# Performance work log

Measured on AMD Instinct MI355X. Metric: run time of the kernel, lower is better.

The kernel has to match this reference:

```python
import jax, jax.numpy as jnp
import numpy as np

N_NODES = 20000
N_EDGES = 320000
IN_F = 168
HID = 256


def gcn_conv(x, W, b, src, dst, ew, n_nodes):
    """PyG GCNConv: symmetric normalization with self-loops (fill 1.0).
    out = D^-1/2 (A + I) D^-1/2 X W^T + b, aggregated at dst (source_to_target).
    """
    xw = x @ W.T  # [N, F_out]
    # degree at target nodes, including self-loop weight 1.0
    deg = jax.ops.segment_sum(ew, dst, num_segments=n_nodes) + 1.0
    dinv = jnp.where(deg > 0, jax.lax.rsqrt(deg), 0.0)
    norm = dinv[src] * ew * dinv[dst]  # [E]
    agg = jax.ops.segment_sum(norm[:, None] * xw[src], dst, num_segments=n_nodes)
    # self-loop contribution: norm_ii = dinv[i]^2
    out = agg + (dinv * dinv)[:, None] * xw
    return out + b


def setup_inputs() -> dict:
    key = jax.random.key(0)
    k = jax.random.split(key, 8)
    x = jax.random.normal(k[0], (N_NODES, IN_F), dtype=jnp.float32)
    edge_index = jax.random.randint(k[1], (2, N_EDGES), 0, N_NODES, dtype=jnp.int64)
    edge_weight = jax.random.uniform(k[2], (N_EDGES,), dtype=jnp.float32)
    # GCN layer weights (PyG Linear: y = x W^T), plus per-layer bias
    s1 = 1.0 / np.sqrt(IN_F)
    s2 = 1.0 / np.sqrt(HID)
    W1 = jax.random.uniform(k[3], (HID, IN_F), minval=-s1, maxval=s1, dtype=jnp.float32)
    b1 = jnp.zeros((HID,), dtype=jnp.float32)
    W2 = jax.random.uniform(k[4], (HID, HID), minval=-s2, maxval=s2, dtype=jnp.float32)
    b2 = jnp.zeros((HID,), dtype=jnp.float32)
    return {"x": x, "edge_index": edge_index, "edge_weight": edge_weight,
            "W1": W1, "b1": b1, "W2": W2, "b2": b2}


def reference(x, edge_index, edge_weight, W1, b1, W2, b2):
    src, dst = edge_index[0], edge_index[1]
    h = gcn_conv(x, W1, b1, src, dst, edge_weight, N_NODES)
    h = jax.nn.relu(h)
    h = gcn_conv(h, W2, b2, src, dst, edge_weight, N_NODES)
    h = jax.nn.relu(h)
    return h
```

## Files before the change

kernel.cpp:

```cpp
#include <hip/hip_runtime.h>

#define N_NODES 20000
#define N_EDGES 320000
#define IN_F    168
#define HID     256
#define K1P     192
#define XS      192
#define NF4     42
#define X4      48

typedef __attribute__((ext_vector_type(8))) short bf16x8;
typedef __attribute__((ext_vector_type(4))) float f32x4;
typedef __attribute__((ext_vector_type(2))) float f32x2;

__device__ __forceinline__ short f2bf(float f) {
    union { float f; unsigned u; } v; v.f = f;
    unsigned r = v.u + 0x7FFFu + ((v.u >> 16) & 1u);
    return (short)(r >> 16);
}
__device__ __forceinline__ f32x2 bfp(unsigned u) {
    f32x2 r;
    r.x = __uint_as_float(u << 16);
    r.y = __uint_as_float(u & 0xFFFF0000u);
    return r;
}

__global__ void prep_all(const float* __restrict__ x, short* __restrict__ xb,
                         const float* __restrict__ W1, const float* __restrict__ W2,
                         short* __restrict__ w1b, short* __restrict__ w2b,
                         const int* __restrict__ ei, const float* __restrict__ ew,
                         float* __restrict__ deg, int* __restrict__ counts) {
    const int xTot  = N_NODES * X4;
    const int w1Tot = 256 * X4;
    const int w2Tot = 256 * 64;
    int i = blockIdx.x * 256 + threadIdx.x;
    if (i < xTot) {
        int n  = i / X4;
        int k4 = i - n * X4;
        short4 o;
        if (k4 < NF4) {
            float4 v = *(const float4*)(x + (size_t)n * IN_F + k4 * 4);
            o = make_short4(f2bf(v.x), f2bf(v.y), f2bf(v.z), f2bf(v.w));
        } else {
            o = make_short4(0, 0, 0, 0);
        }
        *(short4*)(xb + (size_t)n * XS + k4 * 4) = o;
        return;
    }
    i -= xTot;
    if (i < w1Tot) {
        int r  = i / X4;
        int k4 = i - r * X4;
        short4 o;
        if (k4 < NF4) {
            float4 v = *(const float4*)(W1 + (size_t)r * IN_F + k4 * 4);
            o = make_short4(f2bf(v.x), f2bf(v.y), f2bf(v.z), f2bf(v.w));
        } else {
            o = make_short4(0, 0, 0, 0);
        }
        *(short4*)(w1b + (size_t)r * K1P + k4 * 4) = o;
        return;
    }
    i -= w1Tot;
    if (i < w2Tot) {
        int r  = i >> 6;
        int c4 = i & 63;
        float4 v = *(const float4*)(W2 + (size_t)r * HID + c4 * 4);
        *(short4*)(w2b + (size_t)r * HID + c4 * 4) =
            make_short4(f2bf(v.x), f2bf(v.y), f2bf(v.z), f2bf(v.w));
        return;
    }
    i -= w2Tot;
    if (i < N_EDGES) {
        int d = ei[N_EDGES + i];
        atomicAdd(&deg[d], ew[i]);
        atomicAdd(&counts[d], 1);
    }
}


__global__ __launch_bounds__(1024) void scan_part(const int* __restrict__ counts,
                                                  int* __restrict__ offs,
                                                  int* __restrict__ bsum,
                                                  float* __restrict__ deg, int n) {
    int tid  = threadIdx.x;
    int lane = tid & 63;
    int wv   = tid >> 6;
    int i = blockIdx.x * 1024 + tid;
    if (i < n) deg[i] = rsqrtf(deg[i] + 1.0f);
    __shared__ int wsum[16];
    int v = (i < n) ? ((counts[i] + 7) & ~7) : 0;
    int incl = v;
    #pragma unroll
    for (int d = 1; d < 64; d <<= 1) {
        int t = __shfl_up(incl, d);
        if (lane >= d) incl += t;
    }
    if (lane == 63) wsum[wv] = incl;
    __syncthreads();
    if (wv == 0) {
        int w = (lane < 16) ? wsum[lane] : 0;
        int winc = w;
        #pragma unroll
        for (int d = 1; d < 16; d <<= 1) {
            int t = __shfl_up(winc, d);
            if (lane >= d) winc += t;
        }
        if (lane < 16) wsum[lane] = winc - w;
    }
    __syncthreads();
    if (i < n) offs[i] = wsum[wv] + incl - v;
    if (tid == 1023) bsum[blockIdx.x] = wsum[15] + incl;
}

__global__ __launch_bounds__(1024) void scan_add(const int* __restrict__ bsum,
                                                 int* __restrict__ offs, int n) {
    int i = blockIdx.x * 1024 + threadIdx.x;
    int add = 0;
    for (int b = 0; b < (int)blockIdx.x; ++b) add += bsum[b];
    if (i < n) offs[i] += add;
    if (i == n) offs[n] = add + bsum[blockIdx.x];
}

__global__ void scatter_edges(const int* __restrict__ ei, const float* __restrict__ ew,
                              const float* __restrict__ dinv, const int* __restrict__ offs,
                              const int* __restrict__ counts,
                              int* __restrict__ cursor, int2* __restrict__ er) {
    int t = blockIdx.x * 256 + threadIdx.x;
    if (t < N_EDGES) {
        int s = ei[t];
        int d = ei[N_EDGES + t];
        int pos = offs[d] + atomicAdd(&cursor[d], 1);
        float nm = dinv[s] * ew[t] * dinv[d];
        er[pos] = make_int2(s, __float_as_int(nm));
        return;
    }
    int n = t - N_EDGES;
    if (n < N_NODES) {
        int p   = offs[n] + counts[n];
        int end = offs[n + 1];
        for (; p < end; ++p) er[p] = make_int2(0, 0);
    }
}


__global__ __launch_bounds__(256) void agg_x(const short* __restrict__ xb,
                                             const float* __restrict__ dinv,
                                             const int* __restrict__ offs,
                                             const int2* __restrict__ er,
                                             short* __restrict__ ax) {
    int wave = threadIdx.x >> 6;
    int lane = threadIdx.x & 63;
    int n = blockIdx.x * 4 + wave;
    bool act = lane < NF4;
    int lo4 = act ? lane * 4 : 0;
    float di = dinv[n];
    float sw = di * di;
    uint2 sv = *(const uint2*)(xb + (size_t)n * XS + lo4);
    f32x2 a01 = bfp(sv.x) * sw;
    f32x2 a23 = bfp(sv.y) * sw;

    int p0 = offs[n], p1 = offs[n + 1];
    for (int p = p0; p < p1; p += 8) {
        const int4* e4 = (const int4*)(er + p);
        int4 eA = e4[0], eB = e4[1], eC = e4[2], eD = e4[3];
        uint2 r0 = *(const uint2*)(xb + (size_t)eA.x * XS + lo4);
        uint2 r1 = *(const uint2*)(xb + (size_t)eA.z * XS + lo4);
        uint2 r2 = *(const uint2*)(xb + (size_t)eB.x * XS + lo4);
        uint2 r3 = *(const uint2*)(xb + (size_t)eB.z * XS + lo4);
        uint2 r4 = *(const uint2*)(xb + (size_t)eC.x * XS + lo4);
        uint2 r5 = *(const uint2*)(xb + (size_t)eC.z * XS + lo4);
        uint2 r6 = *(const uint2*)(xb + (size_t)eD.x * XS + lo4);
        uint2 r7 = *(const uint2*)(xb + (size_t)eD.z * XS + lo4);
        float w0 = __int_as_float(eA.y), w1 = __int_as_float(eA.w);
        float w2 = __int_as_float(eB.y), w3 = __int_as_float(eB.w);
        float w4 = __int_as_float(eC.y), w5 = __int_as_float(eC.w);
        float w6 = __int_as_float(eD.y), w7 = __int_as_float(eD.w);
        a01 += bfp(r0.x) * w0; a23 += bfp(r0.y) * w0;
        a01 += bfp(r1.x) * w1; a23 += bfp(r1.y) * w1;
        a01 += bfp(r2.x) * w2; a23 += bfp(r2.y) * w2;
        a01 += bfp(r3.x) * w3; a23 += bfp(r3.y) * w3;
        a01 += bfp(r4.x) * w4; a23 += bfp(r4.y) * w4;
        a01 += bfp(r5.x) * w5; a23 += bfp(r5.y) * w5;
        a01 += bfp(r6.x) * w6; a23 += bfp(r6.y) * w6;
        a01 += bfp(r7.x) * w7; a23 += bfp(r7.y) * w7;
    }

    size_t base = (size_t)n * K1P + lane * 4;
    if (act) {
        *(short4*)&ax[base] = make_short4(f2bf(a01.x), f2bf(a01.y),
                                          f2bf(a23.x), f2bf(a23.y));
    } else if (lane < 48) {
        *(short4*)&ax[base] = make_short4(0, 0, 0, 0);
    }
}

__global__ __launch_bounds__(256) void agg_h(const short* __restrict__ h1h,
                                             const float* __restrict__ dinv,
                                             const int* __restrict__ offs,
                                             const int2* __restrict__ er,
                                             short* __restrict__ ah) {
    int wave = threadIdx.x >> 6;
    int lane = threadIdx.x & 63;
    int n = blockIdx.x * 4 + wave;
    int lo4 = lane * 4;
    float di = dinv[n];
    float sw = di * di;
    uint2 sv = *(const uint2*)(h1h + (size_t)n * HID + lo4);
    f32x2 a01 = bfp(sv.x) * sw;
    f32x2 a23 = bfp(sv.y) * sw;

    int p0 = offs[n], p1 = offs[n + 1];
    for (int p = p0; p < p1; p += 8) {
        const int4* e4 = (const int4*)(er + p);
        int4 eA = e4[0], eB = e4[1], eC = e4[2], eD = e4[3];
        uint2 r0 = *(const uint2*)(h1h + (size_t)eA.x * HID + lo4);
        uint2 r1 = *(const uint2*)(h1h + (size_t)eA.z * HID + lo4);
        uint2 r2 = *(const uint2*)(h1h + (size_t)eB.x * HID + lo4);
        uint2 r3 = *(const uint2*)(h1h + (size_t)eB.z * HID + lo4);
        uint2 r4 = *(const uint2*)(h1h + (size_t)eC.x * HID + lo4);
        uint2 r5 = *(const uint2*)(h1h + (size_t)eC.z * HID + lo4);
        uint2 r6 = *(const uint2*)(h1h + (size_t)eD.x * HID + lo4);
        uint2 r7 = *(const uint2*)(h1h + (size_t)eD.z * HID + lo4);
        float w0 = __int_as_float(eA.y), w1 = __int_as_float(eA.w);
        float w2 = __int_as_float(eB.y), w3 = __int_as_float(eB.w);
        float w4 = __int_as_float(eC.y), w5 = __int_as_float(eC.w);
        float w6 = __int_as_float(eD.y), w7 = __int_as_float(eD.w);
        a01 += bfp(r0.x) * w0; a23 += bfp(r0.y) * w0;
        a01 += bfp(r1.x) * w1; a23 += bfp(r1.y) * w1;
        a01 += bfp(r2.x) * w2; a23 += bfp(r2.y) * w2;
        a01 += bfp(r3.x) * w3; a23 += bfp(r3.y) * w3;
        a01 += bfp(r4.x) * w4; a23 += bfp(r4.y) * w4;
        a01 += bfp(r5.x) * w5; a23 += bfp(r5.y) * w5;
        a01 += bfp(r6.x) * w6; a23 += bfp(r6.y) * w6;
        a01 += bfp(r7.x) * w7; a23 += bfp(r7.y) * w7;
    }

    *(short4*)&ah[(size_t)n * HID + lo4] = make_short4(f2bf(a01.x), f2bf(a01.y),
                                                       f2bf(a23.x), f2bf(a23.y));
}


#define LDS_STRIDE 72

__global__ __launch_bounds__(256) void gemm_bf(const short* __restrict__ Ah,
                                               const short* __restrict__ Wh,
                                               const float* __restrict__ bias,
                                               float* __restrict__ Cf,
                                               short* __restrict__ Cbf,
                                               int M, int Ks, int nsteps, int mode) {
    __shared__ short sAh[64 * LDS_STRIDE];
    __shared__ short sWh[64 * LDS_STRIDE];

    const int idx   = blockIdx.x;
    const int group = idx >> 5;
    const int xcd   = idx & 7;
    const int slot  = (idx >> 3) & 3;
    const int mt    = group * 8 + xcd;
    const int mtiles = (M + 63) >> 6;
    if (mt >= mtiles) return;
    const int bm = mt * 64;
    const int bn = slot * 64;

    const int tid  = threadIdx.x;
    const int lane = tid & 63;
    const int wv   = tid >> 6;
    const int l16  = lane & 15;
    const int quad = lane >> 4;
    const int wm   = (wv & 1) * 32;
    const int wn   = (wv >> 1) * 32;

    const int srow = tid >> 2;
    const int sseg = (tid & 3) * 16;
    int arow = bm + srow; if (arow >= M) arow = M - 1;
    const short* gAh = Ah + (size_t)arow * Ks;
    const short* gWh = Wh + (size_t)(bn + srow) * Ks;
    const int lds_off = srow * LDS_STRIDE + sseg;

    f32x4 acc00 = {0,0,0,0}, acc01 = {0,0,0,0}, acc10 = {0,0,0,0}, acc11 = {0,0,0,0};

    int4 pah0 = *(const int4*)(gAh + sseg), pah1 = *(const int4*)(gAh + sseg + 8);
    int4 pwh0 = *(const int4*)(gWh + sseg), pwh1 = *(const int4*)(gWh + sseg + 8);

    for (int ks = 0; ks < nsteps; ++ks) {
        *(int4*)&sAh[lds_off] = pah0; *(int4*)&sAh[lds_off + 8] = pah1;
        *(int4*)&sWh[lds_off] = pwh0; *(int4*)&sWh[lds_off + 8] = pwh1;
        __syncthreads();
        if (ks + 1 < nsteps) {
            int o = (ks + 1) * 64 + sseg;
            pah0 = *(const int4*)(gAh + o); pah1 = *(const int4*)(gAh + o + 8);
            pwh0 = *(const int4*)(gWh + o); pwh1 = *(const int4*)(gWh + o + 8);
        }
        #pragma unroll
        for (int o = 0; o < 2; ++o) {
            const int a0 = (wm + l16) * LDS_STRIDE + o * 32 + quad * 8;
            const int a1 = a0 + 16 * LDS_STRIDE;
            const int w0 = (wn + l16) * LDS_STRIDE + o * 32 + quad * 8;
            const int w1 = w0 + 16 * LDS_STRIDE;
            bf16x8 ah0 = *(const bf16x8*)&sAh[a0];
            bf16x8 ah1 = *(const bf16x8*)&sAh[a1];
            bf16x8 wh0 = *(const bf16x8*)&sWh[w0];
            bf16x8 wh1 = *(const bf16x8*)&sWh[w1];
            acc00 = __builtin_amdgcn_mfma_f32_16x16x32_bf16(ah0, wh0, acc00, 0, 0, 0);
            acc01 = __builtin_amdgcn_mfma_f32_16x16x32_bf16(ah0, wh1, acc01, 0, 0, 0);
            acc10 = __builtin_amdgcn_mfma_f32_16x16x32_bf16(ah1, wh0, acc10, 0, 0, 0);
            acc11 = __builtin_amdgcn_mfma_f32_16x16x32_bf16(ah1, wh1, acc11, 0, 0, 0);
        }
        __syncthreads();
    }

    const int colb = bn + wn + l16;
    const int rowb = bm + wm + quad * 4;
    const float b0 = bias[colb];
    const float b1 = bias[colb + 16];
    #pragma unroll
    for (int r = 0; r < 4; ++r) {
        int row = rowb + r;
        if (row < M) {
            float v0 = acc00[r] + b0; v0 = v0 > 0.f ? v0 : 0.f;
            float v1 = acc01[r] + b1; v1 = v1 > 0.f ? v1 : 0.f;
            if (mode == 0) {
                Cbf[(size_t)row * HID + colb]      = f2bf(v0);
                Cbf[(size_t)row * HID + colb + 16] = f2bf(v1);
            } else {
                Cf[(size_t)row * HID + colb]      = v0;
                Cf[(size_t)row * HID + colb + 16] = v1;
            }
        }
        int row2 = row + 16;
        if (row2 < M) {
            float v0 = acc10[r] + b0; v0 = v0 > 0.f ? v0 : 0.f;
            float v1 = acc11[r] + b1; v1 = v1 > 0.f ? v1 : 0.f;
            if (mode == 0) {
                Cbf[(size_t)row2 * HID + colb]      = f2bf(v0);
                Cbf[(size_t)row2 * HID + colb + 16] = f2bf(v1);
            } else {
                Cf[(size_t)row2 * HID + colb]      = v0;
                Cf[(size_t)row2 * HID + colb + 16] = v1;
            }
        }
    }
}


extern "C" void kernel_launch(void* const* d_in, const int* in_sizes, int n_in,
                              void* d_out, int out_size, void* d_ws, size_t ws_size,
                              hipStream_t stream) {
    const float* x  = (const float*)d_in[0];
    const int*   ei = (const int*)d_in[1];
    const float* ew = (const float*)d_in[2];
    const float* W1 = (const float*)d_in[3];
    const float* b1 = (const float*)d_in[4];
    const float* W2 = (const float*)d_in[5];
    const float* b2 = (const float*)d_in[6];
    float* out = (float*)d_out;

    char* ws = (char*)d_ws;
    float* deg      = (float*)(ws);
    int*   counts   = (int*)(ws + 80000);
    int*   cursor   = (int*)(ws + 160000);
    int*   offs     = (int*)(ws + 240000);
    int*   bsum     = (int*)(ws + 320016);
    int2*  er       = (int2*)(ws + 320144);
    short* ax       = (short*)(ws + 4160144);
    short* ah       = (short*)(ws + 4160144);
    short* h1h      = (short*)(ws + 14400144);
    short* w1b      = (short*)(ws + 24640144);
    short* w2b      = (short*)(ws + 24738448);
    short* xb       = (short*)(ws + 24869520);

    hipMemsetAsync(d_ws, 0, 320144, stream);

    const int prep_tot = N_NODES * X4 + 256 * X4 + 256 * 64 + N_EDGES;
    prep_all<<<(prep_tot + 255) / 256, 256, 0, stream>>>(
        x, xb, W1, W2, w1b, w2b, ei, ew, deg, counts);
    scan_part<<<20, 1024, 0, stream>>>(counts, offs, bsum, deg, N_NODES);
    scan_add<<<20, 1024, 0, stream>>>(bsum, offs, N_NODES);
    const int sc_blocks = (N_EDGES + N_NODES + 255) / 256;
    scatter_edges<<<sc_blocks, 256, 0, stream>>>(ei, ew, deg, offs, counts, cursor, er);

    const int mtiles = (N_NODES + 63) / 64;
    const int gemm_grid = ((mtiles + 7) / 8) * 32;
    agg_x<<<N_NODES / 4, 256, 0, stream>>>(xb, deg, offs, er, ax);
    gemm_bf<<<gemm_grid, 256, 0, stream>>>(ax, w1b, b1, nullptr, h1h,
                                           N_NODES, K1P, 3, 0);
    agg_h<<<N_NODES / 4, 256, 0, stream>>>(h1h, deg, offs, er, ah);
    gemm_bf<<<gemm_grid, 256, 0, stream>>>(ah, w2b, b2, out, nullptr,
                                           N_NODES, HID, 4, 1);
}
```

Baseline: 200.1 us.

## Merge two-pass scan into one block and prefetch edge records in aggregation

Replaces the two-kernel scan with a single 1024-thread block where each thread scans 20 counts serially. The same kernel also zeroes the cursor array, which shrinks the memset. The aggregation loops in agg_x and agg_h now load the next group of 8 edge records before gathering the current rows, so the index load latency overlaps the gathers. The cost is a single-block scan running on one CU and extra registers in the aggregation kernels.

```diff
diff --git a/kernel.cpp b/kernel.cpp
--- a/kernel.cpp
+++ b/kernel.cpp
@@ -78,19 +78,33 @@
     }
 }
 
-
-__global__ __launch_bounds__(1024) void scan_part(const int* __restrict__ counts,
-                                                  int* __restrict__ offs,
-                                                  int* __restrict__ bsum,
-                                                  float* __restrict__ deg, int n) {
-    int tid  = threadIdx.x;
-    int lane = tid & 63;
-    int wv   = tid >> 6;
-    int i = blockIdx.x * 1024 + tid;
-    if (i < n) deg[i] = rsqrtf(deg[i] + 1.0f);
+__global__ __launch_bounds__(1024) void scan1(const int* __restrict__ counts,
+                                              int* __restrict__ offs,
+                                              float* __restrict__ deg,
+                                              int* __restrict__ cursor) {
+    const int tid  = threadIdx.x;
+    const int lane = tid & 63;
+    const int wv   = tid >> 6;
     __shared__ int wsum[16];
-    int v = (i < n) ? ((counts[i] + 7) & ~7) : 0;
-    int incl = v;
+
+    const int base = tid * 20;
+    int loc[20];
+    int s = 0;
+    #pragma unroll
+    for (int j = 0; j < 20; ++j) {
+        int i = base + j;
+        int c = (i < N_NODES) ? ((counts[i] + 7) & ~7) : 0;
+        loc[j] = s; s += c;
+    }
+    #pragma unroll
+    for (int j = 0; j < 20; ++j) {
+        int i = base + j;
+        if (i < N_NODES) {
+            deg[i] = rsqrtf(deg[i] + 1.0f);
+            cursor[i] = 0;
+        }
+    }
+    int incl = s;
     #pragma unroll
     for (int d = 1; d < 64; d <<= 1) {
         int t = __shfl_up(incl, d);
@@ -109,17 +123,13 @@
         if (lane < 16) wsum[lane] = winc - w;
     }
     __syncthreads();
-    if (i < n) offs[i] = wsum[wv] + incl - v;
-    if (tid == 1023) bsum[blockIdx.x] = wsum[15] + incl;
-}
-
-__global__ __launch_bounds__(1024) void scan_add(const int* __restrict__ bsum,
-                                                 int* __restrict__ offs, int n) {
-    int i = blockIdx.x * 1024 + threadIdx.x;
-    int add = 0;
-    for (int b = 0; b < (int)blockIdx.x; ++b) add += bsum[b];
-    if (i < n) offs[i] += add;
-    if (i == n) offs[n] = add + bsum[blockIdx.x];
+    int excl = wsum[wv] + incl - s;
+    #pragma unroll
+    for (int j = 0; j < 20; ++j) {
+        int i = base + j;
+        if (i < N_NODES) offs[i] = excl + loc[j];
+    }
+    if (tid == 1023) offs[N_NODES] = excl + s;
 }
 
 __global__ void scatter_edges(const int* __restrict__ ei, const float* __restrict__ ew,
@@ -161,29 +171,34 @@
     f32x2 a23 = bfp(sv.y) * sw;
 
     int p0 = offs[n], p1 = offs[n + 1];
-    for (int p = p0; p < p1; p += 8) {
-        const int4* e4 = (const int4*)(er + p);
-        int4 eA = e4[0], eB = e4[1], eC = e4[2], eD = e4[3];
-        uint2 r0 = *(const uint2*)(xb + (size_t)eA.x * XS + lo4);
-        uint2 r1 = *(const uint2*)(xb + (size_t)eA.z * XS + lo4);
-        uint2 r2 = *(const uint2*)(xb + (size_t)eB.x * XS + lo4);
-        uint2 r3 = *(const uint2*)(xb + (size_t)eB.z * XS + lo4);
-        uint2 r4 = *(const uint2*)(xb + (size_t)eC.x * XS + lo4);
-        uint2 r5 = *(const uint2*)(xb + (size_t)eC.z * XS + lo4);
-        uint2 r6 = *(const uint2*)(xb + (size_t)eD.x * XS + lo4);
-        uint2 r7 = *(const uint2*)(xb + (size_t)eD.z * XS + lo4);
-        float w0 = __int_as_float(eA.y), w1 = __int_as_float(eA.w);
-        float w2 = __int_as_float(eB.y), w3 = __int_as_float(eB.w);
-        float w4 = __int_as_float(eC.y), w5 = __int_as_float(eC.w);
-        float w6 = __int_as_float(eD.y), w7 = __int_as_float(eD.w);
-        a01 += bfp(r0.x) * w0; a23 += bfp(r0.y) * w0;
-        a01 += bfp(r1.x) * w1; a23 += bfp(r1.y) * w1;
-        a01 += bfp(r2.x) * w2; a23 += bfp(r2.y) * w2;
-        a01 += bfp(r3.x) * w3; a23 += bfp(r3.y) * w3;
-        a01 += bfp(r4.x) * w4; a23 += bfp(r4.y) * w4;
-        a01 += bfp(r5.x) * w5; a23 += bfp(r5.y) * w5;
-        a01 += bfp(r6.x) * w6; a23 += bfp(r6.y) * w6;
-        a01 += bfp(r7.x) * w7; a23 += bfp(r7.y) * w7;
+    if (p0 < p1) {
+        const int4* c4 = (const int4*)(er + p0);
+        int4 eA = c4[0], eB = c4[1], eC = c4[2], eD = c4[3];
+        for (int p = p0 + 8; p <= p1; p += 8) {
+            const int4* n4 = (const int4*)(er + (p < p1 ? p : p0));
+            int4 fA = n4[0], fB = n4[1], fC = n4[2], fD = n4[3];
+            uint2 r0 = *(const uint2*)(xb + (size_t)eA.x * XS + lo4);
+            uint2 r1 = *(const uint2*)(xb + (size_t)eA.z * XS + lo4);
+            uint2 r2 = *(const uint2*)(xb + (size_t)eB.x * XS + lo4);
+            uint2 r3 = *(const uint2*)(xb + (size_t)eB.z * XS + lo4);
+            uint2 r4 = *(const uint2*)(xb + (size_t)eC.x * XS + lo4);
+            uint2 r5 = *(const uint2*)(xb + (size_t)eC.z * XS + lo4);
+            uint2 r6 = *(const uint2*)(xb + (size_t)eD.x * XS + lo4);
+            uint2 r7 = *(const uint2*)(xb + (size_t)eD.z * XS + lo4);
+            float w0 = __int_as_float(eA.y), w1 = __int_as_float(eA.w);
+            float w2 = __int_as_float(eB.y), w3 = __int_as_float(eB.w);
+            float w4 = __int_as_float(eC.y), w5 = __int_as_float(eC.w);
+            float w6 = __int_as_float(eD.y), w7 = __int_as_float(eD.w);
+            a01 += bfp(r0.x) * w0; a23 += bfp(r0.y) * w0;
+            a01 += bfp(r1.x) * w1; a23 += bfp(r1.y) * w1;
+            a01 += bfp(r2.x) * w2; a23 += bfp(r2.y) * w2;
+            a01 += bfp(r3.x) * w3; a23 += bfp(r3.y) * w3;
+            a01 += bfp(r4.x) * w4; a23 += bfp(r4.y) * w4;
+            a01 += bfp(r5.x) * w5; a23 += bfp(r5.y) * w5;
+            a01 += bfp(r6.x) * w6; a23 += bfp(r6.y) * w6;
+            a01 += bfp(r7.x) * w7; a23 += bfp(r7.y) * w7;
+            eA = fA; eB = fB; eC = fC; eD = fD;
+        }
     }
 
     size_t base = (size_t)n * K1P + lane * 4;
@@ -211,35 +226,39 @@
     f32x2 a23 = bfp(sv.y) * sw;
 
     int p0 = offs[n], p1 = offs[n + 1];
-    for (int p = p0; p < p1; p += 8) {
-        const int4* e4 = (const int4*)(er + p);
-        int4 eA = e4[0], eB = e4[1], eC = e4[2], eD = e4[3];
-        uint2 r0 = *(const uint2*)(h1h + (size_t)eA.x * HID + lo4);
-        uint2 r1 = *(const uint2*)(h1h + (size_t)eA.z * HID + lo4);
-        uint2 r2 = *(const uint2*)(h1h + (size_t)eB.x * HID + lo4);
-        uint2 r3 = *(const uint2*)(h1h + (size_t)eB.z * HID + lo4);
-        uint2 r4 = *(const uint2*)(h1h + (size_t)eC.x * HID + lo4);
-        uint2 r5 = *(const uint2*)(h1h + (size_t)eC.z * HID + lo4);
-        uint2 r6 = *(const uint2*)(h1h + (size_t)eD.x * HID + lo4);
-        uint2 r7 = *(const uint2*)(h1h + (size_t)eD.z * HID + lo4);
-        float w0 = __int_as_float(eA.y), w1 = __int_as_float(eA.w);
-        float w2 = __int_as_float(eB.y), w3 = __int_as_float(eB.w);
-        float w4 = __int_as_float(eC.y), w5 = __int_as_float(eC.w);
-        float w6 = __int_as_float(eD.y), w7 = __int_as_float(eD.w);
-        a01 += bfp(r0.x) * w0; a23 += bfp(r0.y) * w0;
-        a01 += bfp(r1.x) * w1; a23 += bfp(r1.y) * w1;
-        a01 += bfp(r2.x) * w2; a23 += bfp(r2.y) * w2;
-        a01 += bfp(r3.x) * w3; a23 += bfp(r3.y) * w3;
-        a01 += bfp(r4.x) * w4; a23 += bfp(r4.y) * w4;
-        a01 += bfp(r5.x) * w5; a23 += bfp(r5.y) * w5;
-        a01 += bfp(r6.x) * w6; a23 += bfp(r6.y) * w6;
-        a01 += bfp(r7.x) * w7; a23 += bfp(r7.y) * w7;
+    if (p0 < p1) {
+        const int4* c4 = (const int4*)(er + p0);
+        int4 eA = c4[0], eB = c4[1], eC = c4[2], eD = c4[3];
+        for (int p = p0 + 8; p <= p1; p += 8) {
+            const int4* n4 = (const int4*)(er + (p < p1 ? p : p0));
+            int4 fA = n4[0], fB = n4[1], fC = n4[2], fD = n4[3];
+            uint2 r0 = *(const uint2*)(h1h + (size_t)eA.x * HID + lo4);
+            uint2 r1 = *(const uint2*)(h1h + (size_t)eA.z * HID + lo4);
+            uint2 r2 = *(const uint2*)(h1h + (size_t)eB.x * HID + lo4);
+            uint2 r3 = *(const uint2*)(h1h + (size_t)eB.z * HID + lo4);
+            uint2 r4 = *(const uint2*)(h1h + (size_t)eC.x * HID + lo4);
+            uint2 r5 = *(const uint2*)(h1h + (size_t)eC.z * HID + lo4);
+            uint2 r6 = *(const uint2*)(h1h + (size_t)eD.x * HID + lo4);
+            uint2 r7 = *(const uint2*)(h1h + (size_t)eD.z * HID + lo4);
+            float w0 = __int_as_float(eA.y), w1 = __int_as_float(eA.w);
+            float w2 = __int_as_float(eB.y), w3 = __int_as_float(eB.w);
+            float w4 = __int_as_float(eC.y), w5 = __int_as_float(eC.w);
+            float w6 = __int_as_float(eD.y), w7 = __int_as_float(eD.w);
+            a01 += bfp(r0.x) * w0; a23 += bfp(r0.y) * w0;
+            a01 += bfp(r1.x) * w1; a23 += bfp(r1.y) * w1;
+            a01 += bfp(r2.x) * w2; a23 += bfp(r2.y) * w2;
+            a01 += bfp(r3.x) * w3; a23 += bfp(r3.y) * w3;
+            a01 += bfp(r4.x) * w4; a23 += bfp(r4.y) * w4;
+            a01 += bfp(r5.x) * w5; a23 += bfp(r5.y) * w5;
+            a01 += bfp(r6.x) * w6; a23 += bfp(r6.y) * w6;
+            a01 += bfp(r7.x) * w7; a23 += bfp(r7.y) * w7;
+            eA = fA; eB = fB; eC = fC; eD = fD;
+        }
     }
 
     *(short4*)&ah[(size_t)n * HID + lo4] = make_short4(f2bf(a01.x), f2bf(a01.y),
                                                        f2bf(a23.x), f2bf(a23.y));
 }
-
 
 #define LDS_STRIDE 72
 
@@ -360,7 +379,6 @@
     int*   counts   = (int*)(ws + 80000);
     int*   cursor   = (int*)(ws + 160000);
     int*   offs     = (int*)(ws + 240000);
-    int*   bsum     = (int*)(ws + 320016);
     int2*  er       = (int2*)(ws + 320144);
     short* ax       = (short*)(ws + 4160144);
     short* ah       = (short*)(ws + 4160144);
@@ -369,18 +387,18 @@
     short* w2b      = (short*)(ws + 24738448);
     short* xb       = (short*)(ws + 24869520);
 
-    hipMemsetAsync(d_ws, 0, 320144, stream);
+    hipMemsetAsync(d_ws, 0, 160000, stream);
 
     const int prep_tot = N_NODES * X4 + 256 * X4 + 256 * 64 + N_EDGES;
     prep_all<<<(prep_tot + 255) / 256, 256, 0, stream>>>(
         x, xb, W1, W2, w1b, w2b, ei, ew, deg, counts);
-    scan_part<<<20, 1024, 0, stream>>>(counts, offs, bsum, deg, N_NODES);
-    scan_add<<<20, 1024, 0, stream>>>(bsum, offs, N_NODES);
+    scan1<<<1, 1024, 0, stream>>>(counts, offs, deg, cursor);
     const int sc_blocks = (N_EDGES + N_NODES + 255) / 256;
     scatter_edges<<<sc_blocks, 256, 0, stream>>>(ei, ew, deg, offs, counts, cursor, er);
 
     const int mtiles = (N_NODES + 63) / 64;
     const int gemm_grid = ((mtiles + 7) / 8) * 32;
+
     agg_x<<<N_NODES / 4, 256, 0, stream>>>(xb, deg, offs, er, ax);
     gemm_bf<<<gemm_grid, 256, 0, stream>>>(ax, w1b, b1, nullptr, h1h,
                                            N_NODES, K1P, 3, 0);
```

Result: slower. 238.9 us (+19.3%).
